# Optimization experiments

Hardware: AMD Instinct MI355X
Metric: run time of the kernel (lower is better)

Reference implementation:

```python
import jax, jax.numpy as jnp
import numpy as np

B, C_IN, C_OUT = 2, 64, 64
NLAT_IN, NLON_IN = 181, 360
NLAT_OUT, NLON_OUT = 181, 360
KERNEL_SIZE = 9            # piecewise-linear basis, kernel_shape=(3,4): (3-1)*4+1
NNZ_PER = 24               # sparse neighbor entries per (kernel fn, output latitude)
NNZ = KERNEL_SIZE * NLAT_OUT * NNZ_PER


def setup_inputs() -> dict:
    key = jax.random.key(0)
    ks = jax.random.split(key, 6)
    x = jax.random.normal(ks[0], (B, C_IN, NLAT_IN, NLON_IN), jnp.float32)
    # quadrature-merged, normalized filter values (positive, O(1/support) scale)
    psi_vals = jax.random.uniform(ks[1], (NNZ,), jnp.float32) / NNZ_PER
    # structured sparse pattern: every (kernel, lat_out) pair has NNZ_PER neighbors
    psi_ker = jnp.repeat(jnp.arange(KERNEL_SIZE, dtype=jnp.int32), NLAT_OUT * NNZ_PER)
    psi_lat_out = jnp.tile(jnp.repeat(jnp.arange(NLAT_OUT, dtype=jnp.int32), NNZ_PER), KERNEL_SIZE)
    dlat = jax.random.randint(ks[2], (NNZ,), -1, 2, dtype=jnp.int32)
    psi_lat_in = jnp.clip(psi_lat_out + dlat, 0, NLAT_IN - 1)
    psi_lon_in = jax.random.randint(ks[3], (NNZ,), 0, NLON_IN, dtype=jnp.int32)
    scale = (1.0 / (C_IN * KERNEL_SIZE)) ** 0.5
    weight = scale * jax.random.normal(ks[4], (C_OUT, C_IN, KERNEL_SIZE), jnp.float32)
    bias = jnp.zeros((C_OUT,), jnp.float32)
    return dict(x=x, psi_vals=psi_vals, weight=weight, bias=bias,
                psi_ker=psi_ker, psi_lat_out=psi_lat_out,
                psi_lat_in=psi_lat_in, psi_lon_in=psi_lon_in)


def _disco_contraction(x, psi_vals, psi_ker, psi_lat_out, psi_lat_in, psi_lon_in):
    """Sparse DISCO contraction: y[b,c,k,lat_out,p] = sum_e psi_vals[e] *
    x[b,c,lat_in_e,(lon_in_e + p*pscale) % nlon_in]  for entries with (k_e, lat_out_e).
    Mirrors torch-harmonics' roll-and-sparse-bmm loop over output longitudes."""
    b, c, nlat_in, nlon_in = x.shape
    pscale = nlon_in // NLON_OUT
    xf = x.reshape(b * c, nlat_in, nlon_in)          # [BC, nlat_in, nlon_in]
    seg = psi_ker * NLAT_OUT + psi_lat_out           # [NNZ] segment id = (k, lat_out)
    nseg = KERNEL_SIZE * NLAT_OUT

    def one_shift(p):
        lon = (psi_lon_in + p * pscale) % nlon_in    # rolled longitude per entry
        g = xf[:, psi_lat_in, lon] * psi_vals        # [BC, NNZ] gather-multiply
        return jax.ops.segment_sum(g.T, seg, num_segments=nseg)  # [nseg, BC]

    ys = jax.lax.map(one_shift, jnp.arange(NLON_OUT))            # [NLON_OUT, nseg, BC]
    y = ys.transpose(1, 0, 2).reshape(KERNEL_SIZE, NLAT_OUT, NLON_OUT, b, c)
    return y.transpose(3, 4, 0, 1, 2)                # [B, C_in, K, nlat_out, nlon_out]


def reference(x, psi_vals, weight, bias, psi_ker, psi_lat_out, psi_lat_in, psi_lon_in):
    y = _disco_contraction(x, psi_vals, psi_ker, psi_lat_out, psi_lat_in, psi_lon_in)
    # groups=1: weight is [C_out, C_in, K]
    out = jnp.einsum("bckxy,fck->bfxy", y, weight)
    out = out + bias[None, :, None, None]
    return out
```

## Files before the change

kernel.cpp:

```cpp
#include <hip/hip_runtime.h>


#define NB    2
#define CIN   64
#define COUT  64
#define KS    9
#define NLAT  181
#define NLON  360
#define NPER  24

typedef _Float16 f16;
typedef _Float16 f16x8 __attribute__((ext_vector_type(8)));
typedef float    f32x4 __attribute__((ext_vector_type(4)));
typedef float    f32x2 __attribute__((ext_vector_type(2)));
typedef unsigned int u32;
typedef unsigned short u16;
typedef u32 u32x4 __attribute__((ext_vector_type(4)));

#define ROWB      46080
#define XT_BYTES  ((size_t)NB * NLAT * NLON * 64 * 2)
#define WT_BYTES  (KS * 64 * 64 * 2)
#define NMETA     (KS * NLAT * NPER)
#define XS_BYTES  (3 * ROWB)

#define U0  (NB * NLAT * 180 * 8)
#define G0  ((U0 + 255) / 256)
#define G1  ((KS * 4096 + 255) / 256)
#define G2  ((NMETA + 255) / 256)

__global__ __launch_bounds__(256) void prep_kernel(
    const float* __restrict__ x, const float* __restrict__ weight,
    const float* __restrict__ psi_vals, const int* __restrict__ psi_lat_in,
    const int* __restrict__ psi_lon_in,
    f16* __restrict__ xT, f16* __restrict__ wT, int4* __restrict__ meta)
{
    const int bid = blockIdx.x, tid = threadIdx.x;
    if (bid < G0) {
        const int u = bid * 256 + tid;
        if (u >= U0) return;
        const int ch   = u & 7;
        const int v    = u >> 3;
        const int lon2 = v % 180;
        const int w    = v / 180;
        const int lat  = w % NLAT;
        const int b    = w / NLAT;
        const int lon0 = lon2 * 2;
        const float* src = x + ((size_t)(b * CIN + ch * 8) * NLAT + lat) * NLON + lon0;
        f16x8 v0, v1;
#pragma unroll
        for (int j = 0; j < 8; ++j) {
            const f32x2 lv = *(const f32x2*)&src[(size_t)j * NLAT * NLON];
            v0[j] = (f16)lv[0];
            v1[j] = (f16)lv[1];
        }
        const int pos0 = ch ^ (lon0 & 7);
        f16* xd = xT + ((size_t)(b * NLAT + lat) * NLON + lon0) * 64;
        *(f16x8*)&xd[pos0 * 8]            = v0;
        *(f16x8*)&xd[64 + (pos0 ^ 1) * 8] = v1;
        return;
    }
    if (bid < G0 + G1) {
        const int e = (bid - G0) * 256 + tid;
        if (e < KS * 4096) {
            int c = e & 63, f = (e >> 6) & 63, k = e >> 12;
            wT[e] = (f16)weight[((size_t)(f * 64 + c)) * KS + k];
        }
        return;
    }
    {
        const int e = (bid - G0 - G1) * 256 + tid;
        if (e < NMETA) {
            int lat = (e / NPER) % NLAT;
            f16 pvh = (f16)psi_vals[e];
            u32 pb = (u32)__builtin_bit_cast(u16, pvh);
            int lonb = psi_lon_in[e] << 7;
            int4 m;
            m.x = (int)((pb << 16) | pb);
            m.y = (psi_lat_in[e] - lat + 1) * ROWB + lonb;
            m.z = lonb;
            m.w = 0;
            meta[e] = m;
        }
    }
}

__global__ __launch_bounds__(768, 3) void disco_main(
    const f16* __restrict__ xT, const f16* __restrict__ wT,
    const int4* __restrict__ meta, const float* __restrict__ bias,
    float* __restrict__ out)
{
    extern __shared__ char xs[];
    const int tid  = threadIdx.x;
    const int lane = tid & 63, wave = tid >> 6;
    const int pn   = lane & 15, q = lane >> 4;
    const int half2 = blockIdx.x, lat = blockIdx.y, b = blockIdx.z;

    const int tile = half2 * 12 + wave;
    const bool act = tile < 23;
    const int p  = tile * 16 + pn;
    const int pl = p >= NLON ? p - NLON : p;
    const u32 plq  = (u32)((pl << 7) + (q << 4));
    const u32 plqm = plq - (u32)ROWB;
    const u32 thr  = (u32)((NLON - pl) << 7);

    const int rr0 = lat > 0 ? lat - 1 : 0;
    const int rr2 = lat < NLAT - 1 ? lat + 1 : NLAT - 1;

    {
        const size_t bb = (size_t)b * NLAT;
        const f16* s0 = xT + (bb + rr0) * NLON * 64;
        const f16* s1 = xT + (bb + lat) * NLON * 64;
        const f16* s2 = xT + (bb + rr2) * NLON * 64;
        for (int i = tid; i < 2880; i += 768) {
            *(f16x8*)&xs[i * 16]             = *(const f16x8*)&s0[i * 8];
            *(f16x8*)&xs[ROWB + i * 16]      = *(const f16x8*)&s1[i * 8];
            *(f16x8*)&xs[2 * ROWB + i * 16]  = *(const f16x8*)&s2[i * 8];
        }
    }
    __syncthreads();

    f32x4 D[4];
#pragma unroll
    for (int ft = 0; ft < 4; ++ft) D[ft] = (f32x4){0.f, 0.f, 0.f, 0.f};

    if (act) {
        for (int k = 0; k < KS; ++k) {
            f16x8 acc0 = (f16x8){0, 0, 0, 0, 0, 0, 0, 0};
            f16x8 acc1 = (f16x8){0, 0, 0, 0, 0, 0, 0, 0};
            const int4* mp = meta + (k * NLAT + lat) * NPER;
#pragma unroll
            for (int tg = 0; tg < NPER; tg += 4) {
                int4 m[4];
#pragma unroll
                for (int j = 0; j < 4; ++j) m[j] = mp[tg + j];

                u32 a0[4], a1[4];
#pragma unroll
                for (int j = 0; j < 4; ++j) {
                    u32 ad = ((u32)m[j].z >= thr) ? plqm : plq;
                    u32 t  = (u32)m[j].y + ad;
                    u32 a  = t ^ ((t >> 3) & 0x70u);
                    a0[j] = a;
                    a1[j] = a ^ 64u;
                }
                f16x8 xv0[4], xv1[4];
#pragma unroll
                for (int j = 0; j < 4; ++j) xv0[j] = *(const f16x8*)(xs + a0[j]);
#pragma unroll
                for (int j = 0; j < 4; ++j) xv1[j] = *(const f16x8*)(xs + a1[j]);
#pragma unroll
                for (int j = 0; j < 4; ++j) {
                    u32 pk = (u32)m[j].x;
                    u32x4 pkv = {pk, pk, pk, pk};
                    f16x8 pf = __builtin_bit_cast(f16x8, pkv);
                    acc0 += xv0[j] * pf;
                    acc1 += xv1[j] * pf;
                }
            }

            f16x8 Af0[4], Af1[4];
            const f16* wk = wT + (size_t)k * 4096 + q * 8;
#pragma unroll
            for (int ft = 0; ft < 4; ++ft) {
                Af0[ft] = *(const f16x8*)&wk[(ft * 16 + pn) * 64];
                Af1[ft] = *(const f16x8*)&wk[32 + (ft * 16 + pn) * 64];
            }
#pragma unroll
            for (int ft = 0; ft < 4; ++ft) {
                D[ft] = __builtin_amdgcn_mfma_f32_16x16x32_f16(Af0[ft], acc0, D[ft], 0, 0, 0);
                D[ft] = __builtin_amdgcn_mfma_f32_16x16x32_f16(Af1[ft], acc1, D[ft], 0, 0, 0);
            }
        }
    }

    if (act && p < NLON) {
#pragma unroll
        for (int ft = 0; ft < 4; ++ft)
#pragma unroll
            for (int r = 0; r < 4; ++r) {
                const int f = ft * 16 + q * 4 + r;
                out[((size_t)(b * COUT + f) * NLAT + lat) * NLON + p] = D[ft][r] + bias[f];
            }
    }
}

extern "C" void kernel_launch(void* const* d_in, const int* in_sizes, int n_in,
                              void* d_out, int out_size, void* d_ws, size_t ws_size,
                              hipStream_t stream) {
    const float* x          = (const float*)d_in[0];
    const float* psi_vals   = (const float*)d_in[1];
    const float* weight     = (const float*)d_in[2];
    const float* bias       = (const float*)d_in[3];
    const int*   psi_lat_in = (const int*)d_in[6];
    const int*   psi_lon_in = (const int*)d_in[7];
    float* out = (float*)d_out;

    f16*  xT   = (f16*)d_ws;
    f16*  wT   = (f16*)((char*)d_ws + XT_BYTES);
    int4* meta = (int4*)((char*)d_ws + XT_BYTES + WT_BYTES);

    (void)hipFuncSetAttribute((const void*)disco_main,
                              hipFuncAttributeMaxDynamicSharedMemorySize, XS_BYTES);

    prep_kernel<<<dim3(G0 + G1 + G2), 256, 0, stream>>>(
        x, weight, psi_vals, psi_lat_in, psi_lon_in, xT, wT, meta);
    disco_main<<<dim3(2, NLAT, NB), 768, XS_BYTES, stream>>>(
        xT, wT, meta, bias, out);
}
```

Baseline: 195.3 us.

## Split neighbor gathers between global memory and LDS, prefetch compact metadata

```diff
diff --git a/kernel.cpp b/kernel.cpp
--- a/kernel.cpp
+++ b/kernel.cpp
@@ -8,6 +8,8 @@
 #define NLAT  181
 #define NLON  360
 #define NPER  24
+#define NGLB  12
+#define NLDS  12
 
 typedef _Float16 f16;
 typedef _Float16 f16x8 __attribute__((ext_vector_type(8)));
@@ -21,6 +23,7 @@
 #define XT_BYTES  ((size_t)NB * NLAT * NLON * 64 * 2)
 #define WT_BYTES  (KS * 64 * 64 * 2)
 #define NMETA     (KS * NLAT * NPER)
+#define YZ_BYTES  (NMETA * 8)
 #define XS_BYTES  (3 * ROWB)
 
 #define U0  (NB * NLAT * 180 * 8)
@@ -32,7 +35,8 @@
     const float* __restrict__ x, const float* __restrict__ weight,
     const float* __restrict__ psi_vals, const int* __restrict__ psi_lat_in,
     const int* __restrict__ psi_lon_in,
-    f16* __restrict__ xT, f16* __restrict__ wT, int4* __restrict__ meta)
+    f16* __restrict__ xT, f16* __restrict__ wT,
+    int2* __restrict__ yz, u16* __restrict__ pk16)
 {
     const int bid = blockIdx.x, tid = threadIdx.x;
     if (bid < G0) {
@@ -71,23 +75,24 @@
         const int e = (bid - G0 - G1) * 256 + tid;
         if (e < NMETA) {
             int lat = (e / NPER) % NLAT;
+            int t   = e % NPER;
             f16 pvh = (f16)psi_vals[e];
-            u32 pb = (u32)__builtin_bit_cast(u16, pvh);
+            pk16[e] = __builtin_bit_cast(u16, pvh);
             int lonb = psi_lon_in[e] << 7;
-            int4 m;
-            m.x = (int)((pb << 16) | pb);
-            m.y = (psi_lat_in[e] - lat + 1) * ROWB + lonb;
-            m.z = lonb;
-            m.w = 0;
-            meta[e] = m;
+            int2 m;
+            m.y = lonb;
+            m.x = (t < NGLB)
+                ? (psi_lat_in[e] * ROWB + lonb)
+                : ((psi_lat_in[e] - lat + 1) * ROWB + lonb);
+            yz[e] = m;
         }
     }
 }
 
 __global__ __launch_bounds__(768, 3) void disco_main(
     const f16* __restrict__ xT, const f16* __restrict__ wT,
-    const int4* __restrict__ meta, const float* __restrict__ bias,
-    float* __restrict__ out)
+    const int2* __restrict__ yz, const u16* __restrict__ pk16,
+    const float* __restrict__ bias, float* __restrict__ out)
 {
     extern __shared__ char xs[];
     const int tid  = threadIdx.x;
@@ -105,6 +110,7 @@
 
     const int rr0 = lat > 0 ? lat - 1 : 0;
     const int rr2 = lat < NLAT - 1 ? lat + 1 : NLAT - 1;
+    const char* xgb = (const char*)xT + (size_t)b * ((size_t)NLAT * ROWB);
 
     {
         const size_t bb = (size_t)b * NLAT;
@@ -117,6 +123,18 @@
             *(f16x8*)&xs[2 * ROWB + i * 16]  = *(const f16x8*)&s2[i * 8];
         }
     }
+
+    int2 yzb[NPER];
+    u32  pkw[NPER / 2];
+    {
+        const int2* yzp = yz + (size_t)lat * NPER;
+        const u32*  pkp = (const u32*)(pk16 + (size_t)lat * NPER);
+#pragma unroll
+        for (int j = 0; j < NPER; ++j) yzb[j] = yzp[j];
+#pragma unroll
+        for (int j = 0; j < NPER / 2; ++j) pkw[j] = pkp[j];
+    }
+
     __syncthreads();
 
     f32x4 D[4];
@@ -124,46 +142,76 @@
     for (int ft = 0; ft < 4; ++ft) D[ft] = (f32x4){0.f, 0.f, 0.f, 0.f};
 
     if (act) {
+#pragma unroll 1
         for (int k = 0; k < KS; ++k) {
-            f16x8 acc0 = (f16x8){0, 0, 0, 0, 0, 0, 0, 0};
-            f16x8 acc1 = (f16x8){0, 0, 0, 0, 0, 0, 0, 0};
-            const int4* mp = meta + (k * NLAT + lat) * NPER;
-#pragma unroll
-            for (int tg = 0; tg < NPER; tg += 4) {
-                int4 m[4];
-#pragma unroll
-                for (int j = 0; j < 4; ++j) m[j] = mp[tg + j];
-
-                u32 a0[4], a1[4];
-#pragma unroll
-                for (int j = 0; j < 4; ++j) {
-                    u32 ad = ((u32)m[j].z >= thr) ? plqm : plq;
-                    u32 t  = (u32)m[j].y + ad;
-                    u32 a  = t ^ ((t >> 3) & 0x70u);
-                    a0[j] = a;
-                    a1[j] = a ^ 64u;
-                }
-                f16x8 xv0[4], xv1[4];
-#pragma unroll
-                for (int j = 0; j < 4; ++j) xv0[j] = *(const f16x8*)(xs + a0[j]);
-#pragma unroll
-                for (int j = 0; j < 4; ++j) xv1[j] = *(const f16x8*)(xs + a1[j]);
-#pragma unroll
-                for (int j = 0; j < 4; ++j) {
-                    u32 pk = (u32)m[j].x;
-                    u32x4 pkv = {pk, pk, pk, pk};
-                    f16x8 pf = __builtin_bit_cast(f16x8, pkv);
-                    acc0 += xv0[j] * pf;
-                    acc1 += xv1[j] * pf;
-                }
-            }
-
+            const int kn = (k < KS - 1) ? (k + 1) : 0;
+
+            u32 aG[NGLB], aL[NLDS];
+#pragma unroll
+            for (int j = 0; j < NGLB; ++j) {
+                u32 ad = ((u32)yzb[j].y >= thr) ? plqm : plq;
+                u32 t  = (u32)yzb[j].x + ad;
+                aG[j]  = t ^ ((t >> 3) & 0x70u);
+            }
+#pragma unroll
+            for (int j = 0; j < NLDS; ++j) {
+                u32 ad = ((u32)yzb[NGLB + j].y >= thr) ? plqm : plq;
+                u32 t  = (u32)yzb[NGLB + j].x + ad;
+                aL[j]  = t ^ ((t >> 3) & 0x70u);
+            }
+            {
+                const int2* yzp = yz + ((size_t)kn * NLAT + lat) * NPER;
+#pragma unroll
+                for (int j = 0; j < NPER; ++j) yzb[j] = yzp[j];
+            }
+
+            f16x8 xg0[NGLB], xg1[NGLB];
+#pragma unroll
+            for (int j = 0; j < NGLB; ++j) {
+                xg0[j] = *(const f16x8*)(xgb + aG[j]);
+                xg1[j] = *(const f16x8*)(xgb + (aG[j] ^ 64u));
+            }
             f16x8 Af0[4], Af1[4];
             const f16* wk = wT + (size_t)k * 4096 + q * 8;
 #pragma unroll
             for (int ft = 0; ft < 4; ++ft) {
                 Af0[ft] = *(const f16x8*)&wk[(ft * 16 + pn) * 64];
                 Af1[ft] = *(const f16x8*)&wk[32 + (ft * 16 + pn) * 64];
+            }
+            f16x8 xv0[NLDS], xv1[NLDS];
+#pragma unroll
+            for (int j = 0; j < NLDS; ++j) {
+                xv0[j] = *(const f16x8*)(xs + aL[j]);
+                xv1[j] = *(const f16x8*)(xs + (aL[j] ^ 64u));
+            }
+
+            f16x8 acc0 = (f16x8){0, 0, 0, 0, 0, 0, 0, 0};
+            f16x8 acc1 = (f16x8){0, 0, 0, 0, 0, 0, 0, 0};
+#pragma unroll
+            for (int j = 0; j < NGLB; ++j) {
+                u32 w  = pkw[j >> 1];
+                u32 pk = (j & 1) ? ((w & 0xffff0000u) | (w >> 16))
+                                 : ((w << 16) | (w & 0xffffu));
+                u32x4 pkv = {pk, pk, pk, pk};
+                f16x8 pf = __builtin_bit_cast(f16x8, pkv);
+                acc0 += xg0[j] * pf;
+                acc1 += xg1[j] * pf;
+            }
+#pragma unroll
+            for (int j = 0; j < NLDS; ++j) {
+                const int t = NGLB + j;
+                u32 w  = pkw[t >> 1];
+                u32 pk = (t & 1) ? ((w & 0xffff0000u) | (w >> 16))
+                                 : ((w << 16) | (w & 0xffffu));
+                u32x4 pkv = {pk, pk, pk, pk};
+                f16x8 pf = __builtin_bit_cast(f16x8, pkv);
+                acc0 += xv0[j] * pf;
+                acc1 += xv1[j] * pf;
+            }
+            {
+                const u32* pkp = (const u32*)(pk16 + ((size_t)kn * NLAT + lat) * NPER);
+#pragma unroll
+                for (int j = 0; j < NPER / 2; ++j) pkw[j] = pkp[j];
             }
 #pragma unroll
             for (int ft = 0; ft < 4; ++ft) {
@@ -197,13 +245,14 @@
 
     f16*  xT   = (f16*)d_ws;
     f16*  wT   = (f16*)((char*)d_ws + XT_BYTES);
-    int4* meta = (int4*)((char*)d_ws + XT_BYTES + WT_BYTES);
+    int2* yzm  = (int2*)((char*)d_ws + XT_BYTES + WT_BYTES);
+    u16*  pk16 = (u16*)((char*)d_ws + XT_BYTES + WT_BYTES + YZ_BYTES);
 
     (void)hipFuncSetAttribute((const void*)disco_main,
                               hipFuncAttributeMaxDynamicSharedMemorySize, XS_BYTES);
 
     prep_kernel<<<dim3(G0 + G1 + G2), 256, 0, stream>>>(
-        x, weight, psi_vals, psi_lat_in, psi_lon_in, xT, wT, meta);
+        x, weight, psi_vals, psi_lat_in, psi_lon_in, xT, wT, yzm, pk16);
     disco_main<<<dim3(2, NLAT, NB), 768, XS_BYTES, stream>>>(
-        xT, wT, meta, bias, out);
+        xT, wT, yzm, pk16, bias, out);
 }
```

After: 266.7 us. 1.37x slower.
